# Kernel optimization log

Measured on AMD Instinct MI355X. Metric: run time of the kernel, lower is better.

Reference implementation:

```python
import jax, jax.numpy as jnp
import numpy as np

N, D, IN, OUT, K = 50000, 16, 256, 128, 4  # nodes, sampled degree, input_size, output_size, heads
LEAKY_SLOPE = 0.01  # torch F.leaky_relu default


def setup_inputs() -> dict:
    key = jax.random.key(0)
    k1, k2, k3, k4 = jax.random.split(key, 4)
    X = jax.random.normal(k1, (N, IN), dtype=jnp.float32)
    W = jax.random.normal(k2, (K, OUT, IN), dtype=jnp.float32) * 0.05
    a = jax.random.normal(k3, (K, 2 * OUT), dtype=jnp.float32) * 0.05
    neighbor_idx = jax.random.randint(k4, (N, D), 0, N)  # fixed-degree neighbor sample
    return {"X": X, "W": W, "a": a, "neighbor_idx": neighbor_idx}


def reference(X, W, a, neighbor_idx):
    # X: [N, IN]; W: [K, OUT, IN]; a: [K, 2*OUT]; neighbor_idx: [N, D]
    out_dim = W.shape[1]
    # Per-head linear map of every node once: Wh[k, n] = W[k] @ X[n]
    Wh = jnp.einsum('koi,ni->kno', W, X)                       # [K, N, OUT]
    # a splits: first OUT weights multiply mapped neighbour, second OUT multiply mapped self
    a_nb, a_self = a[:, :out_dim], a[:, out_dim:]
    e_nb = jnp.einsum('kno,ko->kn', Wh, a_nb)                  # [K, N] score contribution as a neighbour
    e_self = jnp.einsum('kno,ko->kn', Wh, a_self)              # [K, N] score contribution as center node
    # Edge logits: e[k, i, d] = leaky_relu(a_nb.Wh[j] + a_self.Wh[i]), j = neighbor_idx[i, d]
    e = jax.nn.leaky_relu(e_nb[:, neighbor_idx] + e_self[:, :, None], LEAKY_SLOPE)  # [K, N, D]
    alpha = jax.nn.softmax(e, axis=-1)                         # softmax over each node's neighbour set
    Wh_nb = jnp.take(Wh, neighbor_idx, axis=1)                 # [K, N, D, OUT] gathered neighbour features
    h = jnp.einsum('knd,kndo->kno', alpha, Wh_nb)              # [K, N, OUT] attention-weighted aggregate
    # Concatenate heads along feature dim, matching per-node head-concat in the torch loop
    return jnp.transpose(h, (1, 0, 2)).reshape(X.shape[0], -1)  # [N, K*OUT]
```

## Files before the change

### kernel.cpp

```cpp
#include <hip/hip_runtime.h>

#define N_NODES 50000
#define D_NB 16
#define IN_DIM 256
#define OUT_DIM 128
#define K_HEADS 4
#define SLOPE 0.01f
#define NSLICE 16
#define SLICE_COLS 32

typedef __attribute__((ext_vector_type(8))) short short8;
typedef __attribute__((ext_vector_type(4))) float f32x4;
typedef __attribute__((ext_vector_type(2))) unsigned u32x2;

static __device__ __forceinline__ unsigned f2bf(float f) {
    unsigned u = __float_as_uint(f);
    unsigned r = u + 0x7fffu + ((u >> 16) & 1u);
    return r >> 16;
}
static __device__ __forceinline__ float bf2f(unsigned short b) {
    return __uint_as_float(((unsigned)b) << 16);
}

__global__ __launch_bounds__(256) void prep_w_kernel(
    const float* __restrict__ W, const float* __restrict__ a,
    unsigned short* __restrict__ Wb, float* __restrict__ wt8)
{
    if (blockIdx.x < 2048) {
        const int id = blockIdx.x * 256 + threadIdx.x;
        Wb[id] = (unsigned short)f2bf(W[id]);
        return;
    }
    const int i = threadIdx.x;
    #pragma unroll
    for (int k = 0; k < K_HEADS; ++k) {
        float s0 = 0.f, s1 = 0.f;
        for (int o = 0; o < OUT_DIM; ++o) {
            const float w = W[((size_t)k * OUT_DIM + o) * IN_DIM + i];
            s0 += w * a[k * 2 * OUT_DIM + o];
            s1 += w * a[k * 2 * OUT_DIM + OUT_DIM + o];
        }
        wt8[(k * 2 + 0) * IN_DIM + i] = s0;
        wt8[(k * 2 + 1) * IN_DIM + i] = s1;
    }
}

__global__ __launch_bounds__(256) void prep_kernel(
    const float* __restrict__ X, const float* __restrict__ wt8,
    unsigned short* __restrict__ Xb, float* __restrict__ e_nb, float* __restrict__ e_self)
{
    const int t = threadIdx.x;
    const int w = t >> 6;
    const int lane = t & 63;
    const int n = blockIdx.x * 4 + w;

    const f32x4 x = __builtin_nontemporal_load(
        (const f32x4*)(X + (size_t)n * IN_DIM + lane * 4));
    uint2 pk;
    pk.x = f2bf(x[0]) | (f2bf(x[1]) << 16);
    pk.y = f2bf(x[2]) | (f2bf(x[3]) << 16);
    *(uint2*)(Xb + (size_t)n * IN_DIM + lane * 4) = pk;

    float p[8];
    #pragma unroll
    for (int v = 0; v < 8; ++v) {
        const float4 wv = *(const float4*)(wt8 + v * IN_DIM + lane * 4);
        p[v] = x[0] * wv.x + x[1] * wv.y + x[2] * wv.z + x[3] * wv.w;
    }
    #pragma unroll
    for (int sh = 32; sh >= 1; sh >>= 1) {
        #pragma unroll
        for (int v = 0; v < 8; ++v) p[v] += __shfl_xor(p[v], sh);
    }
    if (lane < 8) {
        const int k = lane >> 1;
        float* dst = (lane & 1) ? e_self : e_nb;
        dst[(size_t)k * N_NODES + n] = p[lane];
    }
}

__global__ __launch_bounds__(256) void agg_kernel(
    const int* __restrict__ nidx, const unsigned short* __restrict__ Xb,
    const float* __restrict__ e_nb, const float* __restrict__ e_self,
    unsigned short* __restrict__ aggX, int n0, int nc)
{
    const int t = threadIdx.x;
    const int w = t >> 6;
    const int lane = t & 63;
    const int n = n0 + blockIdx.x * 4 + w;
    if (n >= n0 + nc || n >= N_NODES) return;

    const int k = lane >> 4;
    const int dl = lane & 15;

    const int nbr = __builtin_nontemporal_load(nidx + (size_t)n * D_NB + dl);
    const float x = e_nb[(size_t)k * N_NODES + nbr] + e_self[(size_t)k * N_NODES + n];
    const float v = x > 0.f ? x : SLOPE * x;
    float m = v;
    #pragma unroll
    for (int sh = 8; sh >= 1; sh >>= 1) m = fmaxf(m, __shfl_xor(m, sh, 16));
    const float pz = __expf(v - m);
    float sum = pz;
    #pragma unroll
    for (int sh = 8; sh >= 1; sh >>= 1) sum += __shfl_xor(sum, sh, 16);
    const float alpha = pz / sum;

    float acc[4][4] = {};
    #pragma unroll
    for (int h = 0; h < 2; ++h) {
        uint2 u[8];
        #pragma unroll
        for (int b = 0; b < 8; ++b) {
            const int nd = __shfl(nbr, h * 8 + b);
            u[b] = *(const uint2*)(Xb + (size_t)nd * IN_DIM + lane * 4);
        }
        #pragma unroll
        for (int b = 0; b < 8; ++b) {
            const float x0 = bf2f((unsigned short)(u[b].x & 0xffffu));
            const float x1 = bf2f((unsigned short)(u[b].x >> 16));
            const float x2 = bf2f((unsigned short)(u[b].y & 0xffffu));
            const float x3 = bf2f((unsigned short)(u[b].y >> 16));
            #pragma unroll
            for (int kk = 0; kk < 4; ++kk) {
                const float ad = __shfl(alpha, kk * 16 + h * 8 + b);
                acc[kk][0] += ad * x0;
                acc[kk][1] += ad * x1;
                acc[kk][2] += ad * x2;
                acc[kk][3] += ad * x3;
            }
        }
    }
    #pragma unroll
    for (int kk = 0; kk < 4; ++kk) {
        uint2 pk;
        pk.x = f2bf(acc[kk][0]) | (f2bf(acc[kk][1]) << 16);
        pk.y = f2bf(acc[kk][2]) | (f2bf(acc[kk][3]) << 16);
        *(uint2*)(aggX + ((size_t)kk * nc + (n - n0)) * IN_DIM + lane * 4) = pk;
    }
}

__global__ __launch_bounds__(512) void gemm2_kernel(
    const unsigned short* __restrict__ aggX, const unsigned short* __restrict__ Wb,
    float* __restrict__ out, int n0, int nc)
{
    __shared__ unsigned short Wlds[2][SLICE_COLS * IN_DIM];

    const int t = threadIdx.x;
    const int lane = t & 63;
    const int w = t >> 6;
    const int lrow = lane & 15;
    const int lk = lane >> 4;
    const int m0 = n0 + blockIdx.x * 128 + w * 16;

    const int arow = m0 + lrow;
    const bool avalid = (arow < n0 + nc) && (arow < N_NODES);

    auto STAGE = [&](int st, int buf) {
        const unsigned short* WbS = Wb + (size_t)st * SLICE_COLS * IN_DIM;
        #pragma unroll
        for (int i = 0; i < 2; ++i) {
            const int c = i * 512 + t;
            const int r = c >> 5;
            const int p = c & 31;
            const int cu = p ^ (r & 7);
            const unsigned short* gsrc = WbS + r * IN_DIM + cu * 8;
            unsigned short* ldst = &Wlds[buf][c * 8];
            __builtin_amdgcn_global_load_lds(
                (const __attribute__((address_space(1))) void*)gsrc,
                (__attribute__((address_space(3))) void*)ldst, 16, 0, 0);
        }
    };

    short8 af[8];
    STAGE(0, 0);
    __syncthreads();

    for (int st = 0; st < NSLICE; ++st) {
        const int buf = st & 1;
        if (st + 1 < NSLICE) STAGE(st + 1, buf ^ 1);

        if ((st & 3) == 0) {
            const unsigned short* Ar = aggX
                + ((size_t)(st >> 2) * nc + (arow - n0)) * IN_DIM + lk * 8;
            #pragma unroll
            for (int kk = 0; kk < 8; ++kk)
                af[kk] = avalid ? *(const short8*)(Ar + kk * 32)
                                : short8{0, 0, 0, 0, 0, 0, 0, 0};
        }

        f32x4 acc[2] = {};
        #pragma unroll
        for (int kk = 0; kk < 8; ++kk) {
            #pragma unroll
            for (int nt = 0; nt < 2; ++nt) {
                const int row = nt * 16 + lrow;
                const int pos = (kk * 4 + lk) ^ (row & 7);
                const short8 bf = *(const short8*)(&Wlds[buf][row * IN_DIM + pos * 8]);
                acc[nt] = __builtin_amdgcn_mfma_f32_16x16x32_bf16(bf, af[kk], acc[nt], 0, 0, 0);
            }
        }

        const int k = st >> 2, cb = st & 3;
        if (avalid) {
            const size_t cbase = (size_t)arow * (K_HEADS * OUT_DIM)
                               + (size_t)k * OUT_DIM + cb * SLICE_COLS + lk * 4;
            #pragma unroll
            for (int nt = 0; nt < 2; ++nt)
                __builtin_nontemporal_store(acc[nt], (f32x4*)(out + cbase + nt * 16));
        }
        __syncthreads();
    }
}

extern "C" void kernel_launch(void* const* d_in, const int* in_sizes, int n_in,
                              void* d_out, int out_size, void* d_ws, size_t ws_size,
                              hipStream_t stream) {
    const float* X = (const float*)d_in[0];
    const float* W = (const float*)d_in[1];
    const float* a = (const float*)d_in[2];
    const int* nidx = (const int*)d_in[3];
    float* out = (float*)d_out;

    const size_t WbB  = (size_t)K_HEADS * OUT_DIM * IN_DIM * 2;
    const size_t XbB  = (size_t)N_NODES * IN_DIM * 2;
    const size_t wt8B = (size_t)8 * IN_DIM * 4;
    const size_t eB   = (size_t)K_HEADS * N_NODES * 4;
    auto need = [&](int nc) {
        return WbB + XbB + wt8B + 2 * eB + (size_t)K_HEADS * nc * IN_DIM * 2 + 1024;
    };

    int np, nc;
    if      (ws_size >= need(50000)) { np = 1; nc = 50000; }
    else if (ws_size >= need(25000)) { np = 2; nc = 25000; }
    else                             { np = 4; nc = 12500; }

    char* p = (char*)d_ws;
    unsigned short* Wb   = (unsigned short*)p;   p += WbB;
    unsigned short* Xb   = (unsigned short*)p;   p += XbB;
    float*          wt8  = (float*)p;            p += wt8B;
    float*          enb  = (float*)p;            p += eB;
    float*          esf  = (float*)p;            p += eB;
    unsigned short* aggX = (unsigned short*)p;

    hipLaunchKernelGGL(prep_w_kernel, dim3(2049), dim3(256), 0, stream, W, a, Wb, wt8);

    hipLaunchKernelGGL(prep_kernel,
        dim3(N_NODES / 4), dim3(256), 0, stream, X, wt8, Xb, enb, esf);

    for (int pass = 0; pass < np; ++pass) {
        const int nb0 = pass * nc;
        hipLaunchKernelGGL(agg_kernel,
            dim3((nc + 3) / 4), dim3(256), 0, stream, nidx, Xb, enb, esf, aggX, nb0, nc);
        hipLaunchKernelGGL(gemm2_kernel,
            dim3((nc + 127) / 128), dim3(512), 0, stream, aggX, Wb, out, nb0, nc);
    }
}
```

Measured before the change: 166.5 us.

## Split weight prep, interleave edge scores per node, prefetch GEMM A fragments

The combined weight-prep kernel becomes two kernels. One converts W to bf16. The other computes the eight folded attention vectors, one block per vector instead of a single block looping over all heads. Edge-score arrays move from head-major to node-major float4 layout, so aggregation fetches one 16-byte vector per neighbour. The GEMM kernel double-buffers the A-operand fragments to prefetch the next head's aggregated rows during the current slice, is fully unrolled, and uses regular stores instead of nontemporal ones. The costs are more registers for the second fragment buffer and one extra kernel launch.

Result: faster. 160.1 us (-3.9%).

```diff
diff --git a/kernel.cpp b/kernel.cpp
--- a/kernel.cpp
+++ b/kernel.cpp
@@ -11,7 +11,6 @@
 
 typedef __attribute__((ext_vector_type(8))) short short8;
 typedef __attribute__((ext_vector_type(4))) float f32x4;
-typedef __attribute__((ext_vector_type(2))) unsigned u32x2;
 
 static __device__ __forceinline__ unsigned f2bf(float f) {
     unsigned u = __float_as_uint(f);
@@ -22,32 +21,30 @@
     return __uint_as_float(((unsigned)b) << 16);
 }
 
-__global__ __launch_bounds__(256) void prep_w_kernel(
-    const float* __restrict__ W, const float* __restrict__ a,
-    unsigned short* __restrict__ Wb, float* __restrict__ wt8)
-{
-    if (blockIdx.x < 2048) {
-        const int id = blockIdx.x * 256 + threadIdx.x;
-        Wb[id] = (unsigned short)f2bf(W[id]);
-        return;
-    }
+__global__ __launch_bounds__(256) void wb_kernel(
+    const float* __restrict__ W, unsigned short* __restrict__ Wb)
+{
+    const int id = blockIdx.x * 256 + threadIdx.x;
+    Wb[id] = (unsigned short)f2bf(W[id]);
+}
+
+__global__ __launch_bounds__(256) void wt8_kernel(
+    const float* __restrict__ W, const float* __restrict__ a, float* __restrict__ wt8)
+{
+    const int v = blockIdx.x;
+    const int k = v >> 1, s = v & 1;
     const int i = threadIdx.x;
-    #pragma unroll
-    for (int k = 0; k < K_HEADS; ++k) {
-        float s0 = 0.f, s1 = 0.f;
-        for (int o = 0; o < OUT_DIM; ++o) {
-            const float w = W[((size_t)k * OUT_DIM + o) * IN_DIM + i];
-            s0 += w * a[k * 2 * OUT_DIM + o];
-            s1 += w * a[k * 2 * OUT_DIM + OUT_DIM + o];
-        }
-        wt8[(k * 2 + 0) * IN_DIM + i] = s0;
-        wt8[(k * 2 + 1) * IN_DIM + i] = s1;
-    }
+    const float* av = a + k * 2 * OUT_DIM + s * OUT_DIM;
+    float acc = 0.f;
+    #pragma unroll 4
+    for (int o = 0; o < OUT_DIM; ++o)
+        acc += W[((size_t)k * OUT_DIM + o) * IN_DIM + i] * av[o];
+    wt8[v * IN_DIM + i] = acc;
 }
 
 __global__ __launch_bounds__(256) void prep_kernel(
     const float* __restrict__ X, const float* __restrict__ wt8,
-    unsigned short* __restrict__ Xb, float* __restrict__ e_nb, float* __restrict__ e_self)
+    unsigned short* __restrict__ Xb, float* __restrict__ e_nb4, float* __restrict__ e_self4)
 {
     const int t = threadIdx.x;
     const int w = t >> 6;
@@ -72,16 +69,15 @@
         #pragma unroll
         for (int v = 0; v < 8; ++v) p[v] += __shfl_xor(p[v], sh);
     }
-    if (lane < 8) {
-        const int k = lane >> 1;
-        float* dst = (lane & 1) ? e_self : e_nb;
-        dst[(size_t)k * N_NODES + n] = p[lane];
+    if (lane == 0) {
+        *(float4*)(e_nb4 + (size_t)n * 4)   = float4{p[0], p[2], p[4], p[6]};
+        *(float4*)(e_self4 + (size_t)n * 4) = float4{p[1], p[3], p[5], p[7]};
     }
 }
 
 __global__ __launch_bounds__(256) void agg_kernel(
     const int* __restrict__ nidx, const unsigned short* __restrict__ Xb,
-    const float* __restrict__ e_nb, const float* __restrict__ e_self,
+    const float* __restrict__ e_nb4, const float* __restrict__ e_self4,
     unsigned short* __restrict__ aggX, int n0, int nc)
 {
     const int t = threadIdx.x;
@@ -94,7 +90,11 @@
     const int dl = lane & 15;
 
     const int nbr = __builtin_nontemporal_load(nidx + (size_t)n * D_NB + dl);
-    const float x = e_nb[(size_t)k * N_NODES + nbr] + e_self[(size_t)k * N_NODES + n];
+    const float4 eb4 = *(const float4*)(e_nb4 + (size_t)nbr * 4);
+    const float4 es4 = *(const float4*)(e_self4 + (size_t)n * 4);
+    const float en = (k & 2) ? ((k & 1) ? eb4.w : eb4.z) : ((k & 1) ? eb4.y : eb4.x);
+    const float es = (k & 2) ? ((k & 1) ? es4.w : es4.z) : ((k & 1) ? es4.y : es4.x);
+    const float x = en + es;
     const float v = x > 0.f ? x : SLOPE * x;
     float m = v;
     #pragma unroll
@@ -171,23 +171,27 @@
         }
     };
 
-    short8 af[8];
+    short8 af[2][8];
+    auto LOADAF = [&](int head, int slot) {
+        const unsigned short* Ar = aggX + ((size_t)head * nc + (arow - n0)) * IN_DIM + lk * 8;
+        #pragma unroll
+        for (int kk = 0; kk < 8; ++kk)
+            af[slot][kk] = avalid ? *(const short8*)(Ar + kk * 32)
+                                  : short8{0, 0, 0, 0, 0, 0, 0, 0};
+    };
+
     STAGE(0, 0);
+    LOADAF(0, 0);
     __syncthreads();
 
+    #pragma unroll
     for (int st = 0; st < NSLICE; ++st) {
         const int buf = st & 1;
         if (st + 1 < NSLICE) STAGE(st + 1, buf ^ 1);
-
-        if ((st & 3) == 0) {
-            const unsigned short* Ar = aggX
-                + ((size_t)(st >> 2) * nc + (arow - n0)) * IN_DIM + lk * 8;
-            #pragma unroll
-            for (int kk = 0; kk < 8; ++kk)
-                af[kk] = avalid ? *(const short8*)(Ar + kk * 32)
-                                : short8{0, 0, 0, 0, 0, 0, 0, 0};
-        }
-
+        if ((st & 3) == 3 && st + 1 < NSLICE)
+            LOADAF((st >> 2) + 1, ((st >> 2) + 1) & 1);
+
+        const int slot = (st >> 2) & 1;
         f32x4 acc[2] = {};
         #pragma unroll
         for (int kk = 0; kk < 8; ++kk) {
@@ -196,7 +200,7 @@
                 const int row = nt * 16 + lrow;
                 const int pos = (kk * 4 + lk) ^ (row & 7);
                 const short8 bf = *(const short8*)(&Wlds[buf][row * IN_DIM + pos * 8]);
-                acc[nt] = __builtin_amdgcn_mfma_f32_16x16x32_bf16(bf, af[kk], acc[nt], 0, 0, 0);
+                acc[nt] = __builtin_amdgcn_mfma_f32_16x16x32_bf16(bf, af[slot][kk], acc[nt], 0, 0, 0);
             }
         }
 
@@ -206,7 +210,7 @@
                                + (size_t)k * OUT_DIM + cb * SLICE_COLS + lk * 4;
             #pragma unroll
             for (int nt = 0; nt < 2; ++nt)
-                __builtin_nontemporal_store(acc[nt], (f32x4*)(out + cbase + nt * 16));
+                *(f32x4*)(out + cbase + nt * 16) = acc[nt];
         }
         __syncthreads();
     }
@@ -238,19 +242,20 @@
     unsigned short* Wb   = (unsigned short*)p;   p += WbB;
     unsigned short* Xb   = (unsigned short*)p;   p += XbB;
     float*          wt8  = (float*)p;            p += wt8B;
-    float*          enb  = (float*)p;            p += eB;
-    float*          esf  = (float*)p;            p += eB;
+    float*          enb4 = (float*)p;            p += eB;
+    float*          esf4 = (float*)p;            p += eB;
     unsigned short* aggX = (unsigned short*)p;
 
-    hipLaunchKernelGGL(prep_w_kernel, dim3(2049), dim3(256), 0, stream, W, a, Wb, wt8);
+    hipLaunchKernelGGL(wb_kernel, dim3(2048), dim3(256), 0, stream, W, Wb);
+    hipLaunchKernelGGL(wt8_kernel, dim3(8), dim3(256), 0, stream, W, a, wt8);
 
     hipLaunchKernelGGL(prep_kernel,
-        dim3(N_NODES / 4), dim3(256), 0, stream, X, wt8, Xb, enb, esf);
+        dim3(N_NODES / 4), dim3(256), 0, stream, X, wt8, Xb, enb4, esf4);
 
     for (int pass = 0; pass < np; ++pass) {
         const int nb0 = pass * nc;
         hipLaunchKernelGGL(agg_kernel,
-            dim3((nc + 3) / 4), dim3(256), 0, stream, nidx, Xb, enb, esf, aggX, nb0, nc);
+            dim3((nc + 3) / 4), dim3(256), 0, stream, nidx, Xb, enb4, esf4, aggX, nb0, nc);
         hipLaunchKernelGGL(gemm2_kernel,
             dim3((nc + 127) / 128), dim3(512), 0, stream, aggX, Wb, out, nb0, nc);
     }
```
